# Kernel tuning notes

Hardware: AMD Instinct MI355X
Metric: run time of the kernel (lower is better)

Reference implementation:

```python
import jax, jax.numpy as jnp
import numpy as np
import math

CH_IN = 256
NUM_HEADS = 4
HEAD_CH = 64
NUM_GROUPS = 32
EPS = 1e-5


def setup_inputs() -> dict:
    key = jax.random.key(0)
    ks = jax.random.split(key, 12)
    B, C, H, W = 16, CH_IN, 32, 32
    s_in = 1.0 / math.sqrt(C)  # conv 1x1 fan_in init scale
    s_proj = 1.0 / math.sqrt(NUM_HEADS * HEAD_CH)
    return {
        "x": jax.random.normal(ks[0], (B, C, H, W), dtype=jnp.float32),
        "gamma": jnp.ones((C,), dtype=jnp.float32),
        "beta": jnp.zeros((C,), dtype=jnp.float32),
        # per-head 1x1 convs stacked: [num_heads, head_ch, ch_in]
        "wq": jax.random.normal(ks[1], (NUM_HEADS, HEAD_CH, C), dtype=jnp.float32) * s_in,
        "bq": jax.random.normal(ks[2], (NUM_HEADS, HEAD_CH), dtype=jnp.float32) * s_in,
        "wk": jax.random.normal(ks[3], (NUM_HEADS, HEAD_CH, C), dtype=jnp.float32) * s_in,
        "bk": jax.random.normal(ks[4], (NUM_HEADS, HEAD_CH), dtype=jnp.float32) * s_in,
        "wv": jax.random.normal(ks[5], (NUM_HEADS, HEAD_CH, C), dtype=jnp.float32) * s_in,
        "bv": jax.random.normal(ks[6], (NUM_HEADS, HEAD_CH), dtype=jnp.float32) * s_in,
        # output 1x1 conv: [ch_in, num_heads*head_ch]
        "wproj": jax.random.normal(ks[7], (C, NUM_HEADS * HEAD_CH), dtype=jnp.float32) * s_proj,
        "bproj": jax.random.normal(ks[8], (C,), dtype=jnp.float32) * s_proj,
    }


def group_norm(x, gamma, beta):
    B, C, H, W = x.shape
    xg = x.reshape(B, NUM_GROUPS, C // NUM_GROUPS, H, W)
    mean = xg.mean(axis=(2, 3, 4), keepdims=True)
    var = xg.var(axis=(2, 3, 4), keepdims=True)
    xn = (xg - mean) * jax.lax.rsqrt(var + EPS)
    xn = xn.reshape(B, C, H, W)
    return xn * gamma[None, :, None, None] + beta[None, :, None, None]


def reference(x, gamma, beta, wq, bq, wk, bk, wv, bv, wproj, bproj):
    B, C, H, W = x.shape
    L = H * W
    h = group_norm(x, gamma, beta)
    hf = h.reshape(B, C, L)  # [B, C, L]
    # per-head 1x1 convs as batched channel contractions: [B, n_heads, d, L]
    q = jnp.einsum("bcl,ndc->bndl", hf, wq) + bq[None, :, :, None]
    k = jnp.einsum("bcl,ndc->bndl", hf, wk) + bk[None, :, :, None]
    v = jnp.einsum("bcl,ndc->bndl", hf, wv) + bv[None, :, :, None]
    scale = 1.0 / math.sqrt(HEAD_CH)
    scores = jnp.einsum("bndl,bndm->bnlm", q, k) * scale  # [B, n, L, L]
    attn = jax.nn.softmax(scores, axis=-1)
    out = jnp.einsum("bnlm,bndm->bndl", attn, v)  # [B, n, d, L]
    out = out.reshape(B, NUM_HEADS * HEAD_CH, L)  # concat heads along channels
    proj = jnp.einsum("bel,ce->bcl", out, wproj) + bproj[None, :, None]
    return proj.reshape(B, C, H, W) + x
```

## Files before the change

### kernel.cpp

```cpp
#include <hip/hip_runtime.h>
#include <hip/hip_bf16.h>
#include <stdint.h>


typedef __hip_bfloat16 bf16;
typedef __attribute__((ext_vector_type(8))) short short8;
typedef __attribute__((ext_vector_type(4))) float float4v;
typedef __attribute__((ext_vector_type(16))) float float16v;

#if __has_builtin(__builtin_amdgcn_exp2f)
#define EXP2F(x) __builtin_amdgcn_exp2f(x)
#else
#define EXP2F(x) exp2f(x)
#endif

__device__ __forceinline__ float max3f(float a, float b, float c) {
  return fmaxf(fmaxf(a, b), c);
}
__device__ __forceinline__ unsigned int cvtpk(float lo, float hi) {
  unsigned int pk;
  asm("v_cvt_pk_bf16_f32 %0, %1, %2" : "=v"(pk) : "v"(lo), "v"(hi));
  return pk;
}

__device__ __forceinline__ int qk_fidx(int d, int l) {
  return ((((l >> 5) * 4 + (d >> 4)) * 64 + ((d >> 3) & 1) * 32 + (l & 31)) << 3) + (d & 7);
}
__device__ __forceinline__ int v_fidx(int d, int l) {
  return (((((((l >> 5) * 2 + (d >> 5)) * 2 + ((l >> 4) & 1)) * 2 + ((l >> 3) & 1)) * 32) + (d & 31)) << 3) + (l & 7);
}

__global__ __launch_bounds__(256) void stats_wpack_kernel(
    const float* __restrict__ x, float2* __restrict__ stats,
    const float* __restrict__ wq, const float* __restrict__ wk,
    const float* __restrict__ wv, const float* __restrict__ wp,
    bf16* __restrict__ Wb, bf16* __restrict__ Pb) {
  if (blockIdx.x < 512) {
    int b = blockIdx.x >> 5, g = blockIdx.x & 31;
    const float4* xp4 = (const float4*)(x + (size_t)(b * 256 + g * 8) * 1024);
    float s = 0.f, ss = 0.f;
    for (int i = threadIdx.x; i < 2048; i += 256) {
      float4 v = xp4[i];
      s  += (v.x + v.y) + (v.z + v.w);
      ss += (v.x * v.x + v.y * v.y) + (v.z * v.z + v.w * v.w);
    }
    #pragma unroll
    for (int o = 32; o; o >>= 1) { s += __shfl_down(s, o); ss += __shfl_down(ss, o); }
    __shared__ float red[2][4];
    int wid = threadIdx.x >> 6;
    if ((threadIdx.x & 63) == 0) { red[0][wid] = s; red[1][wid] = ss; }
    __syncthreads();
    if (threadIdx.x == 0) {
      s  = red[0][0] + red[0][1] + red[0][2] + red[0][3];
      ss = red[1][0] + red[1][1] + red[1][2] + red[1][3];
      float mean = s * (1.f / 8192.f);
      float var  = ss * (1.f / 8192.f) - mean * mean;
      stats[blockIdx.x] = make_float2(mean, rsqrtf(var + 1e-5f));
    }
  } else {
    int i = (blockIdx.x - 512) * 256 + threadIdx.x;
    if (i < 196608) {
      int r = i >> 8, c = i & 255;
      const float* src = (r < 256) ? wq : (r < 512) ? wk : wv;
      Wb[i] = __float2bfloat16(src[(r & 255) * 256 + c]);
    } else {
      int j2 = i - 196608;
      int jj = j2 & 7, lane2 = (j2 >> 3) & 63;
      int kk2 = (j2 >> 9) & 15, w2 = j2 >> 13;
      int m = w2 * 32 + (lane2 & 31);
      int e = kk2 * 16 + (lane2 >> 5) * 8 + jj;
      Pb[j2] = __float2bfloat16(wp[m * 256 + e]);
    }
  }
}

__global__ __launch_bounds__(256) void gemm_qkv_fused(
    const float* __restrict__ x, const float* __restrict__ gamma,
    const float* __restrict__ beta, const float2* __restrict__ stats,
    const bf16* __restrict__ Wb,
    const float* __restrict__ bq, const float* __restrict__ bk,
    const float* __restrict__ bv,
    bf16* __restrict__ qkv, size_t qkv_bstride, int b_off) {
  __shared__ bf16 As[128][40];
  __shared__ bf16 Bs[128][40];
  __shared__ float2 ssh[256];
  int zb = blockIdx.z, b = zb + b_off;
  int m0 = blockIdx.y * 128, l0 = blockIdx.x * 128;
  const float* xb = x + (size_t)b * 262144;
  int tid = threadIdx.x, lane = tid & 63, wave = tid >> 6;
  int l16 = lane & 15, quad = lane >> 4;
  int mi0 = (wave & 1) * 4, nj0 = (wave >> 1) * 4;

  {
    float2 st = stats[b * 32 + (tid >> 3)];
    float sc = st.y * gamma[tid];
    ssh[tid] = make_float2(sc, beta[tid] - st.x * sc);
  }

  float4v acc[4][4];
  #pragma unroll
  for (int i = 0; i < 4; i++)
    #pragma unroll
    for (int j = 0; j < 4; j++) acc[i][j] = (float4v){0.f, 0.f, 0.f, 0.f};

  for (int kc = 0; kc < 8; kc++) {
    __syncthreads();
    #pragma unroll
    for (int it = 0; it < 2; it++) {
      int s = it * 256 + tid;
      int mm = s >> 2, kk = (s & 3) * 8;
      *(short8*)&As[mm][kk] = *(const short8*)&Wb[(size_t)(m0 + mm) * 256 + kc * 32 + kk];
    }
    #pragma unroll
    for (int it = 0; it < 4; it++) {
      int s = it * 256 + tid;
      int ll = s & 127, cg = s >> 7;
      int c = kc * 32 + cg * 4;
      float2 sh0 = ssh[c], sh1 = ssh[c + 1], sh2 = ssh[c + 2], sh3 = ssh[c + 3];
      const float* xp = &xb[(size_t)c * 1024 + l0 + ll];
      float v0 = xp[0]    * sh0.x + sh0.y;
      float v1 = xp[1024] * sh1.x + sh1.y;
      float v2 = xp[2048] * sh2.x + sh2.y;
      float v3 = xp[3072] * sh3.x + sh3.y;
      uint2 pk;
      pk.x = cvtpk(v0, v1);
      pk.y = cvtpk(v2, v3);
      *(uint2*)&Bs[ll][cg * 4] = pk;
    }
    __syncthreads();
    short8 af[4], bfr[4];
    #pragma unroll
    for (int i = 0; i < 4; i++) af[i]  = *(const short8*)&As[(mi0 + i) * 16 + l16][quad * 8];
    #pragma unroll
    for (int j = 0; j < 4; j++) bfr[j] = *(const short8*)&Bs[(nj0 + j) * 16 + l16][quad * 8];
    #pragma unroll
    for (int i = 0; i < 4; i++)
      #pragma unroll
      for (int j = 0; j < 4; j++)
        acc[i][j] = __builtin_amdgcn_mfma_f32_16x16x32_bf16(af[i], bfr[j], acc[i][j], 0, 0, 0);
  }

  bf16* Cp = qkv + (size_t)zb * qkv_bstride;
  int sec = m0 >> 8;
  const float* bptr = (sec == 0) ? bq : (sec == 1) ? bk : bv;
  if (sec <= 1) {
    float osc = (sec == 0) ? 0.125f * 1.4426950408889634f : 1.0f;
    bf16* Tp = Cp + sec * 262144;
    #pragma unroll
    for (int i = 0; i < 4; i++) {
      int rrb = (m0 & 255) + (mi0 + i) * 16 + quad * 4;
      int nh = rrb >> 6, d0 = rrb & 63;
      float b0 = bptr[rrb], b1 = bptr[rrb + 1], b2 = bptr[rrb + 2], b3 = bptr[rrb + 3];
      bf16* Tph = Tp + nh * 65536;
      #pragma unroll
      for (int j = 0; j < 4; j++) {
        int l = l0 + (nj0 + j) * 16 + l16;
        uint2 pk;
        pk.x = cvtpk((acc[i][j][0] + b0) * osc, (acc[i][j][1] + b1) * osc);
        pk.y = cvtpk((acc[i][j][2] + b2) * osc, (acc[i][j][3] + b3) * osc);
        *(uint2*)&Tph[qk_fidx(d0, l)] = pk;
      }
    }
  } else {
    bf16* Vfp = Cp + 524288;
    #pragma unroll
    for (int i = 0; i < 4; i++)
      #pragma unroll
      for (int rp = 0; rp < 2; rp++) {
        int rr = (m0 & 255) + (mi0 + i) * 16 + quad * 4 + rp * 2;
        int nh = rr >> 6, d = rr & 63;
        float b0 = bptr[rr], b1 = bptr[rr + 1];
        bf16* Vfh = Vfp + nh * 65536;
        #pragma unroll
        for (int j = 0; j < 4; j++) {
          int l = l0 + (nj0 + j) * 16 + l16;
          unsigned int pk = cvtpk(acc[i][j][rp * 2] + b0, acc[i][j][rp * 2 + 1] + b1);
          *(unsigned short*)&Vfh[v_fidx(d, l)] = (unsigned short)pk;
          *(unsigned short*)&Vfh[v_fidx(d + 1, l)] = (unsigned short)(pk >> 16);
        }
      }
  }
}

__global__ __launch_bounds__(512) void attn_proj_kernel(
    const bf16* __restrict__ qkv, const bf16* __restrict__ PbF,
    const float* __restrict__ bproj, const float* __restrict__ x,
    float* __restrict__ out, size_t qkv_bstride, int b_off) {
  __shared__ __align__(16) char lds[52736];
  float* OB   = (float*)lds;
  float* mL   = (float*)(lds + 34816);
  float* lL   = (float*)(lds + 35328);
  bf16*  O_lds = (bf16*)(lds + 35840);

  int b, qg;
  {
    int f = blockIdx.x;
    if (gridDim.x == 512) {
      int c = f & 7, t = f >> 3;
      b = ((t & 1) << 3) + c; qg = t >> 1;
    } else {
      b = b_off; qg = f;
    }
  }
  const bf16* base = qkv + (size_t)(gridDim.x == 512 ? b : 0) * qkv_bstride;
  int tid = threadIdx.x;
  int lane = tid & 63, wave = tid >> 6;
  int l31 = lane & 31, hb2 = lane >> 5;
  int n = wave & 3, half = wave >> 2;
  const bf16* Qf = base + n * 65536;
  const bf16* Kf = base + 262144 + n * 65536;
  const bf16* Vf = base + 524288 + n * 65536;

  short8 qb[4];
  #pragma unroll
  for (int ds = 0; ds < 4; ds++)
    qb[ds] = *(const short8*)&Qf[(((qg * 4 + ds) << 6) + lane) << 3];

  float m_run = -1e30f, l_run = 0.f;
  float16v oaccT[2];
  #pragma unroll
  for (int dh = 0; dh < 2; dh++)
    #pragma unroll
    for (int r = 0; r < 16; r++) oaccT[dh][r] = 0.f;

  auto swp = [&](unsigned int a, unsigned int bb, unsigned int& o0, unsigned int& o1) {
#if __has_builtin(__builtin_amdgcn_permlane32_swap)
    auto rr = __builtin_amdgcn_permlane32_swap((int)a, (int)bb, false, false);
    o0 = (unsigned int)rr[0]; o1 = (unsigned int)rr[1];
#else
    unsigned int sa = (unsigned int)__shfl_xor((int)a, 32, 64);
    unsigned int sb = (unsigned int)__shfl_xor((int)bb, 32, 64);
    o0 = hb2 ? sb : a;
    o1 = hb2 ? bb : sa;
#endif
  };

  int k0 = half << 4;
  for (int kt = k0; kt < k0 + 16; kt++) {
    short8 kf[4];
    #pragma unroll
    for (int ds = 0; ds < 4; ds++)
      kf[ds] = *(const short8*)&Kf[(((kt * 4 + ds) << 6) + lane) << 3];
    short8 vf[2][2];
    #pragma unroll
    for (int dh = 0; dh < 2; dh++)
      #pragma unroll
      for (int s = 0; s < 2; s++)
        vf[dh][s] = *(const short8*)&Vf[((((kt * 2 + dh) * 2 + s) << 6) + lane) << 3];

    float16v sacc;
    #pragma unroll
    for (int r = 0; r < 16; r++) sacc[r] = 0.f;
    #pragma unroll
    for (int ds = 0; ds < 4; ds++)
      sacc = __builtin_amdgcn_mfma_f32_32x32x16_bf16(kf[ds], qb[ds], sacc, 0, 0, 0);

    float a0 = max3f(sacc[0], sacc[1], sacc[2]);
    float a1 = max3f(sacc[3], sacc[4], sacc[5]);
    float a2 = max3f(sacc[6], sacc[7], sacc[8]);
    float a3 = max3f(sacc[9], sacc[10], sacc[11]);
    float a4 = max3f(sacc[12], sacc[13], sacc[14]);
    float cmax = fmaxf(max3f(a0, a1, a2), max3f(a3, a4, sacc[15]));
    cmax = fmaxf(cmax, __shfl_xor(cmax, 32, 64));

    if (__any(cmax > m_run + 8.f)) {
      float mnew = fmaxf(m_run, cmax);
      float alpha = EXP2F(m_run - mnew);
      #pragma unroll
      for (int dh = 0; dh < 2; dh++)
        #pragma unroll
        for (int r = 0; r < 16; r++) oaccT[dh][r] *= alpha;
      l_run *= alpha;
      m_run = mnew;
    }

    float p[16];
    #pragma unroll
    for (int r = 0; r < 16; r++) p[r] = EXP2F(sacc[r] - m_run);
    float s0 = (p[0] + p[1]) + (p[2] + p[3]);
    float s1 = (p[4] + p[5]) + (p[6] + p[7]);
    float s2 = (p[8] + p[9]) + (p[10] + p[11]);
    float s3 = (p[12] + p[13]) + (p[14] + p[15]);
    float psum = (s0 + s1) + (s2 + s3);
    psum += __shfl_xor(psum, 32, 64);
    l_run += psum;

    unsigned int w[8];
    #pragma unroll
    for (int i = 0; i < 8; i++) w[i] = cvtpk(p[2 * i], p[2 * i + 1]);
    short8 pb[2];
    {
      unsigned int o0, o1, o2, o3;
      swp(w[0], w[2], o0, o2); swp(w[1], w[3], o1, o3);
      unsigned int* pw = (unsigned int*)&pb[0];
      pw[0] = o0; pw[1] = o1; pw[2] = o2; pw[3] = o3;
      swp(w[4], w[6], o0, o2); swp(w[5], w[7], o1, o3);
      pw = (unsigned int*)&pb[1];
      pw[0] = o0; pw[1] = o1; pw[2] = o2; pw[3] = o3;
    }

    #pragma unroll
    for (int dh = 0; dh < 2; dh++)
      #pragma unroll
      for (int s = 0; s < 2; s++)
        oaccT[dh] = __builtin_amdgcn_mfma_f32_32x32x16_bf16(vf[dh][s], pb[s], oaccT[dh], 0, 0, 0);
  }

  if (half == 1) {
    float* OBn = OB + n * 2176;
    #pragma unroll
    for (int dh = 0; dh < 2; dh++)
      #pragma unroll
      for (int rq = 0; rq < 4; rq++) {
        float4v t = {oaccT[dh][4 * rq], oaccT[dh][4 * rq + 1],
                     oaccT[dh][4 * rq + 2], oaccT[dh][4 * rq + 3]};
        *(float4v*)&OBn[l31 * 68 + dh * 32 + 8 * rq + 4 * hb2] = t;
      }
    if (hb2 == 0) { mL[n * 32 + l31] = m_run; lL[n * 32 + l31] = l_run; }
  }
  __syncthreads();
  if (half == 0) {
    float mB = mL[n * 32 + l31], lB = lL[n * 32 + l31];
    float ms = fmaxf(m_run, mB);
    float eA = EXP2F(m_run - ms), eB = EXP2F(mB - ms);
    float inv = 1.f / (l_run * eA + lB * eB);
    eA *= inv; eB *= inv;
    const float* OBn = OB + n * 2176 + l31 * 68;
    bf16* orow = O_lds + l31 * 264 + n * 64;
    #pragma unroll
    for (int dh = 0; dh < 2; dh++)
      #pragma unroll
      for (int rp = 0; rp < 8; rp++) {
        int r = rp * 2;
        int d = dh * 32 + (r & 3) + 8 * (r >> 2) + 4 * hb2;
        unsigned int pk = cvtpk(oaccT[dh][r] * eA + OBn[d] * eB,
                                oaccT[dh][r + 1] * eA + OBn[d + 1] * eB);
        *(unsigned int*)&orow[d] = pk;
      }
  }
  __syncthreads();

  float16v pacc;
  #pragma unroll
  for (int r = 0; r < 16; r++) pacc[r] = 0.f;
  #pragma unroll
  for (int kk = 0; kk < 16; kk++) {
    short8 a = *(const short8*)&O_lds[l31 * 264 + kk * 16 + hb2 * 8];
    short8 bb = *(const short8*)&PbF[(((wave * 16 + kk) << 6) + lane) << 3];
    pacc = __builtin_amdgcn_mfma_f32_32x32x16_bf16(a, bb, pacc, 0, 0, 0);
  }
  int m = (wave << 5) + l31;
  float bias = bproj[m];
  const float* xr = x + (((size_t)(b * 256 + m)) << 10) + (qg << 5);
  float* orw = out + (((size_t)(b * 256 + m)) << 10) + (qg << 5);
  #pragma unroll
  for (int rp = 0; rp < 8; rp++) {
    int r = rp * 2;
    int ll = (r & 3) + 8 * (r >> 2) + 4 * hb2;
    float2 xv = *(const float2*)&xr[ll];
    float2 ov;
    ov.x = pacc[r] + bias + xv.x;
    ov.y = pacc[r + 1] + bias + xv.y;
    *(float2*)&orw[ll] = ov;
  }
}

extern "C" void kernel_launch(void* const* d_in, const int* in_sizes, int n_in,
                              void* d_out, int out_size, void* d_ws, size_t ws_size,
                              hipStream_t stream) {
  int ix = 0, iga = 1, ibe = 2, iwq = 3, ibq = 4, iwk = 5, ibk = 6,
      iwv = 7, ibv = 8, iwp = 9, ibp = 10;
  if (in_sizes[0] != 4194304) {
    if (in_sizes[10] == 4194304 && in_sizes[1] == 256) {
      ibe = 0; ibk = 1; ibp = 2; ibq = 3; ibv = 4; iga = 5;
      iwk = 6; iwp = 7; iwq = 8; iwv = 9; ix = 10;
    } else if (in_sizes[10] == 4194304 && in_sizes[1] == 65536) {
      ibp = 0; iwp = 1; ibv = 2; iwv = 3; ibk = 4; iwk = 5;
      ibq = 6; iwq = 7; ibe = 8; iga = 9; ix = 10;
    } else {
      for (int i = 0; i < 11; i++) if (in_sizes[i] == 4194304) ix = i;
    }
  }
  const float* x     = (const float*)d_in[ix];
  const float* gamma = (const float*)d_in[iga];
  const float* beta  = (const float*)d_in[ibe];
  const float* wq    = (const float*)d_in[iwq];
  const float* bq    = (const float*)d_in[ibq];
  const float* wk    = (const float*)d_in[iwk];
  const float* bk    = (const float*)d_in[ibk];
  const float* wv    = (const float*)d_in[iwv];
  const float* bv    = (const float*)d_in[ibv];
  const float* wproj = (const float*)d_in[iwp];
  const float* bproj = (const float*)d_in[ibp];
  float* out = (float*)d_out;

  const size_t QKV_B = (size_t)768 * 1024;
  char* wsp = (char*)d_ws;
  float2* stats = (float2*)wsp;
  bf16* Wb = (bf16*)(wsp + 8192);
  bf16* Pb = (bf16*)(wsp + 8192 + 393216);
  const size_t QKV0 = 8192 + 393216 + 131072;
  size_t full_need = QKV0 + (size_t)16 * QKV_B * 2;

  stats_wpack_kernel<<<1536, 256, 0, stream>>>(x, stats, wq, wk, wv, wproj, Wb, Pb);

  if (ws_size >= full_need) {
    bf16* qkv = (bf16*)(wsp + QKV0);
    gemm_qkv_fused<<<dim3(8, 6, 16), 256, 0, stream>>>(x, gamma, beta, stats, Wb,
                                                       bq, bk, bv, qkv, QKV_B, 0);
    attn_proj_kernel<<<512, 512, 0, stream>>>(qkv, Pb, bproj, x, out, QKV_B, 0);
  } else {
    bf16* qkv = (bf16*)(wsp + QKV0);
    for (int b = 0; b < 16; b++) {
      gemm_qkv_fused<<<dim3(8, 6, 1), 256, 0, stream>>>(x, gamma, beta, stats, Wb,
                                                        bq, bk, bv, qkv, 0, b);
      attn_proj_kernel<<<32, 512, 0, stream>>>(qkv, Pb, bproj, x, out, 0, b);
    }
  }
}
```

Before: 147.1 us.

## Double-buffer K fragment loads in attention loop and remap QKV GEMM grid

The attention inner loop now keeps two K-fragment register sets, loading the next tile's K while the current tile's scores, softmax and PV MMAs run, so global load latency is hidden behind compute. The loop is fully unrolled by pairs. Separately, the QKV GEMM launches as a flat 1D grid of 768 blocks, with a custom index mapping that interleaves batches across consecutive blocks (8 batches per group), likely to spread work across XCDs/L2 better. This raises register pressure and code size in the attention kernel.

```diff
diff --git a/kernel.cpp b/kernel.cpp
--- a/kernel.cpp
+++ b/kernel.cpp
@@ -84,8 +84,18 @@
   __shared__ bf16 As[128][40];
   __shared__ bf16 Bs[128][40];
   __shared__ float2 ssh[256];
-  int zb = blockIdx.z, b = zb + b_off;
-  int m0 = blockIdx.y * 128, l0 = blockIdx.x * 128;
+  int zb, m0, l0;
+  if (gridDim.x == 768) {
+    int f = blockIdx.x;
+    int c = f & 7, t = f >> 3;
+    zb = (t & 1) * 8 + c;
+    int rem = t >> 1;
+    m0 = (rem % 6) * 128;
+    l0 = (rem / 6) * 128;
+  } else {
+    zb = blockIdx.z; m0 = blockIdx.y * 128; l0 = blockIdx.x * 128;
+  }
+  int b = zb + b_off;
   const float* xb = x + (size_t)b * 262144;
   int tid = threadIdx.x, lane = tid & 63, wave = tid >> 6;
   int l16 = lane & 15, quad = lane >> 4;
@@ -235,12 +245,13 @@
 #endif
   };
 
-  int k0 = half << 4;
-  for (int kt = k0; kt < k0 + 16; kt++) {
-    short8 kf[4];
+  auto loadK = [&](short8 (&kf)[4], int kt) {
     #pragma unroll
     for (int ds = 0; ds < 4; ds++)
       kf[ds] = *(const short8*)&Kf[(((kt * 4 + ds) << 6) + lane) << 3];
+  };
+
+  auto step = [&](short8 (&kf)[4], int kt) {
     short8 vf[2][2];
     #pragma unroll
     for (int dh = 0; dh < 2; dh++)
@@ -304,6 +315,17 @@
       #pragma unroll
       for (int s = 0; s < 2; s++)
         oaccT[dh] = __builtin_amdgcn_mfma_f32_32x32x16_bf16(vf[dh][s], pb[s], oaccT[dh], 0, 0, 0);
+  };
+
+  int k0 = half << 4;
+  short8 kfA[4], kfB[4];
+  loadK(kfA, k0);
+  #pragma unroll
+  for (int i = 0; i < 8; i++) {
+    loadK(kfB, k0 + 2 * i + 1);
+    step(kfA, k0 + 2 * i);
+    if (i < 7) loadK(kfA, k0 + 2 * i + 2);
+    step(kfB, k0 + 2 * i + 1);
   }
 
   if (half == 1) {
@@ -406,8 +428,8 @@
 
   if (ws_size >= full_need) {
     bf16* qkv = (bf16*)(wsp + QKV0);
-    gemm_qkv_fused<<<dim3(8, 6, 16), 256, 0, stream>>>(x, gamma, beta, stats, Wb,
-                                                       bq, bk, bv, qkv, QKV_B, 0);
+    gemm_qkv_fused<<<768, 256, 0, stream>>>(x, gamma, beta, stats, Wb,
+                                            bq, bk, bv, qkv, QKV_B, 0);
     attn_proj_kernel<<<512, 512, 0, stream>>>(qkv, Pb, bproj, x, out, QKV_B, 0);
   } else {
     bf16* qkv = (bf16*)(wsp + QKV0);
```

Result: no change. 147.4 us, median of 2 (+0.2%).
